# Kernel optimization log

Measured on AMD Instinct MI355X. Metric: run time of the kernel, lower is better.

## Reference

```python
import jax, jax.numpy as jnp
import numpy as np

T = 4      # num_step (also LSTM num_layers)
R = 64     # num_relation (= LSTM hidden size)
E = 1024   # num_entity
B = 128    # batch
IN = R + 2 * E  # LSTM input size


def _lstm_layer(x_seq, Wih, Whh, bih, bhh):
    # x_seq: [T, B, In]; torch gate order i, f, g, o
    Bsz = x_seq.shape[1]
    H = Whh.shape[1]
    pre = jnp.einsum('tbi,gi->tbg', x_seq, Wih) + bih + bhh  # [T,B,4H]

    def step(carry, z):
        h, c = carry
        z = z + h @ Whh.T
        i, f, g, o = jnp.split(z, 4, axis=-1)
        i, f, o = jax.nn.sigmoid(i), jax.nn.sigmoid(f), jax.nn.sigmoid(o)
        c = f * c + i * jnp.tanh(g)
        h = o * jnp.tanh(c)
        return (h, c), h

    init = (jnp.zeros((Bsz, H), x_seq.dtype), jnp.zeros((Bsz, H), x_seq.dtype))
    _, hs = jax.lax.scan(step, init, pre)
    return hs  # [T, B, H]


def setup_inputs() -> dict:
    key = jax.random.key(0)
    ks = jax.random.split(key, 12)
    s = 0.05
    inp = {
        'x': jax.random.uniform(ks[0], (B, IN), dtype=jnp.float32),
        'kb': jax.random.uniform(ks[1], (R, E, E), dtype=jnp.float32) * 0.01,
        # LSTM layer 0 (input dim IN)
        'Wih0': jax.random.normal(ks[2], (4 * R, IN), dtype=jnp.float32) * s,
        'Whh0': jax.random.normal(ks[3], (4 * R, R), dtype=jnp.float32) * s,
        'bih0': jnp.zeros((4 * R,), jnp.float32),
        'bhh0': jnp.zeros((4 * R,), jnp.float32),
        # LSTM layers 1..T-1 (input dim R)
        'Wih': jax.random.normal(ks[4], (T - 1, 4 * R, R), dtype=jnp.float32) * s,
        'Whh': jax.random.normal(ks[5], (T - 1, 4 * R, R), dtype=jnp.float32) * s,
        'bih': jnp.zeros((T - 1, 4 * R), jnp.float32),
        'bhh': jnp.zeros((T - 1, 4 * R), jnp.float32),
    }
    return inp


def reference(x, kb, Wih0, Whh0, bih0, bhh0, Wih, Whh, bih, bhh):
    # input to LSTM: x repeated T times -> [T, B, IN]
    seq = jnp.broadcast_to(x[None], (T,) + x.shape)
    hs = _lstm_layer(seq, Wih0, Whh0, bih0, bhh0)
    for l in range(T - 1):  # small fixed layer count
        hs = _lstm_layer(hs, Wih[l], Whh[l], bih[l], bhh[l])
    h = jax.nn.softmax(hs, axis=-1)  # [T, B, R] (first softmax)

    mem = [x[:, R:R + E]]  # memory[0] = head entity vector, [B, E]
    for i in range(T):
        h2 = jax.nn.softmax(h[i], axis=-1)  # double softmax, faithful to source
        # causal memory attention over steps k <= i
        att = jax.nn.softmax(jnp.einsum('kbr,br->bk', h[:i + 1], h[i]), axis=-1)  # [B, i+1]
        prev = jnp.einsum('bk,kbe->be', att, jnp.stack(mem))  # [B, E]
        # per-relation operator application: sum_r h2[b,r] * KB[r] @ prev[b]
        tmp = jnp.einsum('ref,bf->bre', kb, prev)  # [B, R, E]
        mem.append(jnp.einsum('br,bre->be', h2, tmp))

    tail = x[:, R + E:R + 2 * E]  # [B, E]
    score = jax.nn.sigmoid(-jnp.einsum('be,be->b', mem[-1], tail))[:, None]  # [B, 1]
    return score
```

## Files before the change

### kernel.cpp

```cpp
#include <hip/hip_runtime.h>
#include <cstdint>
#include <cstddef>

#define B_ 128
#define E_ 1024
#define R_ 64
#define T_ 4
#define IN_ 2112
#define G_ 256

typedef __attribute__((ext_vector_type(4))) float f32x4;
typedef __attribute__((ext_vector_type(8))) __bf16 bf16x8;

__device__ __forceinline__ unsigned short f2bf(float f) {
  unsigned int u = __float_as_uint(f);
  u += 0x7fffu + ((u >> 16) & 1u);
  return (unsigned short)(u >> 16);
}
__device__ __forceinline__ unsigned int pack2(float lo, float hi) {
  return (unsigned int)f2bf(lo) | ((unsigned int)f2bf(hi) << 16);
}
__device__ __forceinline__ float wred_sum(float v) {
#pragma unroll
  for (int m = 32; m > 0; m >>= 1) v += __shfl_xor(v, m, 64);
  return v;
}
__device__ __forceinline__ float wred_max(float v) {
#pragma unroll
  for (int m = 32; m > 0; m >>= 1) v = fmaxf(v, __shfl_xor(v, m, 64));
  return v;
}
__device__ __forceinline__ float fast_sig(float x) {
  return __builtin_amdgcn_rcpf(1.f + __expf(-x));
}
__device__ __forceinline__ float fast_tanh(float x) {
  return 1.f - 2.f * __builtin_amdgcn_rcpf(1.f + __expf(2.f * x));
}

__device__ __forceinline__ void gload_lds16(const void* g, void* l) {
  __builtin_amdgcn_global_load_lds(
      (const __attribute__((address_space(1))) unsigned int*)g,
      (__attribute__((address_space(3))) unsigned int*)l, 16, 0, 0);
}

__global__ __launch_bounds__(256) void fused0_kernel(
    const float* __restrict__ x, const float* __restrict__ kb,
    const float* __restrict__ Wih0, const float* __restrict__ Whh0,
    const float* __restrict__ bih0, const float* __restrict__ bhh0,
    const float* __restrict__ Wih, const float* __restrict__ Whh,
    const float* __restrict__ bih, const float* __restrict__ bhh,
    unsigned short* __restrict__ kb_bf,
    float* __restrict__ part,
    float* __restrict__ h2_out, float* __restrict__ att_out) {
  __shared__ __align__(16) unsigned char smem[20480];
  const int tid = threadIdx.x;
  const int bid = blockIdx.x;

  if (bid >= 128) {
    unsigned short* As = (unsigned short*)smem;
    unsigned short* Bs = As + 128 * 40;
    const int g = bid - 128;
    const int et = g & 7, r = g >> 3;
    const int row = tid >> 1;
    const int c0 = (tid & 1) * 16;
    const float* aptr = x + (size_t)row * IN_ + R_ + c0;
    const float* bptr = kb + (size_t)r * 1048576 + (size_t)(et * 128 + row) * 1024 + c0;
    unsigned short* kdst = kb_bf + (size_t)r * 1048576 + (size_t)(et * 128 + row) * 1024 + c0;
    unsigned short* adst = As + row * 40 + c0;
    unsigned short* bdst = Bs + row * 40 + c0;
    const int wv = tid >> 6, lane = tid & 63;
    const int wm = (wv & 1) * 64, wn = (wv >> 1) * 64;
    const int fr = lane & 15, koff = (lane >> 4) * 8;
    f32x4 acc[4][4];
#pragma unroll
    for (int mt = 0; mt < 4; mt++)
#pragma unroll
      for (int nt = 0; nt < 4; nt++)
#pragma unroll
        for (int q = 0; q < 4; q++) acc[mt][nt][q] = 0.f;

    for (int kk = 0; kk < 32; kk++) {
      const float4 a0 = *(const float4*)(aptr + kk * 32);
      const float4 a1 = *(const float4*)(aptr + kk * 32 + 4);
      const float4 a2 = *(const float4*)(aptr + kk * 32 + 8);
      const float4 a3 = *(const float4*)(aptr + kk * 32 + 12);
      const float4 b0 = *(const float4*)(bptr + kk * 32);
      const float4 b1 = *(const float4*)(bptr + kk * 32 + 4);
      const float4 b2 = *(const float4*)(bptr + kk * 32 + 8);
      const float4 b3 = *(const float4*)(bptr + kk * 32 + 12);
      __syncthreads();
      uint4 u;
      u.x = pack2(a0.x, a0.y); u.y = pack2(a0.z, a0.w);
      u.z = pack2(a1.x, a1.y); u.w = pack2(a1.z, a1.w);
      *(uint4*)adst = u;
      u.x = pack2(a2.x, a2.y); u.y = pack2(a2.z, a2.w);
      u.z = pack2(a3.x, a3.y); u.w = pack2(a3.z, a3.w);
      *(uint4*)(adst + 8) = u;
      uint4 ub;
      ub.x = pack2(b0.x, b0.y); ub.y = pack2(b0.z, b0.w);
      ub.z = pack2(b1.x, b1.y); ub.w = pack2(b1.z, b1.w);
      *(uint4*)bdst = ub;
      *(uint4*)(kdst + kk * 32) = ub;
      ub.x = pack2(b2.x, b2.y); ub.y = pack2(b2.z, b2.w);
      ub.z = pack2(b3.x, b3.y); ub.w = pack2(b3.z, b3.w);
      *(uint4*)(bdst + 8) = ub;
      *(uint4*)(kdst + kk * 32 + 8) = ub;
      __syncthreads();
      bf16x8 af[4], bfr[4];
#pragma unroll
      for (int mt = 0; mt < 4; mt++)
        af[mt] = *(const bf16x8*)(As + (wm + mt * 16 + fr) * 40 + koff);
#pragma unroll
      for (int nt = 0; nt < 4; nt++)
        bfr[nt] = *(const bf16x8*)(Bs + (wn + nt * 16 + fr) * 40 + koff);
#pragma unroll
      for (int mt = 0; mt < 4; mt++)
#pragma unroll
        for (int nt = 0; nt < 4; nt++)
          acc[mt][nt] = __builtin_amdgcn_mfma_f32_16x16x32_bf16(af[mt], bfr[nt], acc[mt][nt], 0, 0, 0);
    }
    const int crow = (lane >> 4) * 4;
    float* pout = part + (size_t)r * 131072;
#pragma unroll
    for (int mt = 0; mt < 4; mt++)
#pragma unroll
      for (int nt = 0; nt < 4; nt++)
#pragma unroll
        for (int q = 0; q < 4; q++)
          pout[(wm + mt * 16 + crow + q) * 1024 + et * 128 + wn + nt * 16 + fr] = acc[mt][nt][q];
    return;
  }

  float* xrow    = (float*)smem;
  float* pre_lds = xrow + IN_;
  float* hbuf    = pre_lds + G_;
  float* zbuf    = hbuf + R_;
  float* hs_out  = zbuf + 2 * G_;
  float* hmat    = hs_out + T_ * R_;

  const int b = bid;
  const int lane = tid & 63, wv = tid >> 6;
  const int s = tid & 63;

  for (int l = tid; l < IN_; l += 256) xrow[l] = x[b * IN_ + l];
  __syncthreads();

  {
    const int gbase = wv * 64;
#pragma unroll 2
    for (int gg = 0; gg < 64; gg++) {
      const float* wr = Wih0 + (size_t)(gbase + gg) * IN_;
      float4 s4 = {0.f, 0.f, 0.f, 0.f};
#pragma unroll
      for (int k = 0; k < 8; k++) {
        float4 w = *(const float4*)(wr + (lane + 64 * k) * 4);
        float4 xv = *(const float4*)(&xrow[(lane + 64 * k) * 4]);
        s4.x += w.x * xv.x; s4.y += w.y * xv.y;
        s4.z += w.z * xv.z; s4.w += w.w * xv.w;
      }
      float part_ = (s4.x + s4.y) + (s4.z + s4.w);
      part_ += wr[2048 + lane] * xrow[2048 + lane];
      float tot = wred_sum(part_);
      if (lane == 0) pre_lds[gbase + gg] = tot;
    }
  }
  float p0 = pre_lds[tid] + bih0[tid] + bhh0[tid];

  float4 w4[16];
  float pret[T_];

  auto scan = [&]() {
    __syncthreads();
    hbuf[s] = 0.f;
    float creg = 0.f;
#pragma unroll
    for (int t = 0; t < T_; t++) {
      float z0 = pret[t], z1 = 0.f, z2 = 0.f, z3 = 0.f;
#pragma unroll
      for (int q = 0; q < 16; q += 4) {
        float4 h0 = *(const float4*)(&hbuf[q * 4]);
        float4 h1 = *(const float4*)(&hbuf[q * 4 + 4]);
        float4 h2v = *(const float4*)(&hbuf[q * 4 + 8]);
        float4 h3 = *(const float4*)(&hbuf[q * 4 + 12]);
        z0 += h0.x * w4[q].x + h0.y * w4[q].y + h0.z * w4[q].z + h0.w * w4[q].w;
        z1 += h1.x * w4[q + 1].x + h1.y * w4[q + 1].y + h1.z * w4[q + 1].z + h1.w * w4[q + 1].w;
        z2 += h2v.x * w4[q + 2].x + h2v.y * w4[q + 2].y + h2v.z * w4[q + 2].z + h2v.w * w4[q + 2].w;
        z3 += h3.x * w4[q + 3].x + h3.y * w4[q + 3].y + h3.z * w4[q + 3].z + h3.w * w4[q + 3].w;
      }
      zbuf[(t & 1) * G_ + tid] = (z0 + z1) + (z2 + z3);
      __syncthreads();
      float iv = fast_sig(zbuf[(t & 1) * G_ + s]);
      float fv = fast_sig(zbuf[(t & 1) * G_ + R_ + s]);
      float gv = fast_tanh(zbuf[(t & 1) * G_ + 2 * R_ + s]);
      float ov = fast_sig(zbuf[(t & 1) * G_ + 3 * R_ + s]);
      creg = fv * creg + iv * gv;
      float h = ov * fast_tanh(creg);
      hbuf[s] = h;
      hs_out[t * R_ + s] = h;
    }
  };

#pragma unroll
  for (int t = 0; t < T_; t++) pret[t] = p0;
#pragma unroll
  for (int q = 0; q < 16; q++)
    w4[q] = *(const float4*)(Whh0 + (size_t)tid * R_ + q * 4);
  scan();

  for (int l = 0; l < T_ - 1; l++) {
#pragma unroll
    for (int q = 0; q < 16; q++)
      w4[q] = *(const float4*)(Wih + ((size_t)l * G_ + tid) * R_ + q * 4);
    const float bsum = bih[l * G_ + tid] + bhh[l * G_ + tid];
#pragma unroll
    for (int t = 0; t < T_; t++) {
      float p = bsum;
#pragma unroll
      for (int q = 0; q < 16; q++) {
        float4 hv = *(const float4*)(&hs_out[t * R_ + q * 4]);
        p += hv.x * w4[q].x + hv.y * w4[q].y + hv.z * w4[q].z + hv.w * w4[q].w;
      }
      pret[t] = p;
    }
#pragma unroll
    for (int q = 0; q < 16; q++)
      w4[q] = *(const float4*)(Whh + ((size_t)l * G_ + tid) * R_ + q * 4);
    scan();
  }

  {
    float v = hs_out[wv * R_ + lane];
    float mx = wred_max(v);
    float ev = expf(v - mx);
    float sm = wred_sum(ev);
    float hval = ev / sm;
    hmat[wv * R_ + lane] = hval;
    float mx2 = wred_max(hval);
    float e2 = expf(hval - mx2);
    float s2 = wred_sum(e2);
    h2_out[(wv * B_ + b) * R_ + lane] = e2 / s2;
    __syncthreads();
    float dots[T_];
    for (int k = 0; k <= wv; k++)
      dots[k] = wred_sum(hmat[k * R_ + lane] * hmat[wv * R_ + lane]);
    if (lane == 0) {
      float mx3 = dots[0];
      for (int k = 1; k <= wv; k++) mx3 = fmaxf(mx3, dots[k]);
      float ss = 0.f, es[T_];
      for (int k = 0; k <= wv; k++) { es[k] = expf(dots[k] - mx3); ss += es[k]; }
      for (int k = 0; k <= wv; k++) att_out[(wv * B_ + b) * 4 + k] = es[k] / ss;
    }
  }
}

__global__ __launch_bounds__(256) void gemm_bf_kernel(
    const unsigned short* __restrict__ Abf,
    const unsigned short* __restrict__ Kbf,
    float* __restrict__ part) {
  __shared__ unsigned short As[2][128 * 32];
  __shared__ unsigned short Bs[2][128 * 32];
  const int tid = threadIdx.x, wv = tid >> 6, lane = tid & 63;
  const int et = blockIdx.x, r = blockIdx.y;
  const int wm = (wv & 1) * 64, wn = (wv >> 1) * 64;
  const int fr = lane & 15, koff = (lane >> 4) * 8;

  const int srow = wv * 32 + (lane >> 2);
  const int scol = (lane & 3) * 8;
  const unsigned short* agp = Abf + (size_t)srow * 1024 + scol;
  const unsigned short* bgp = Kbf + (size_t)r * 1048576 + (size_t)(et * 128 + srow) * 1024 + scol;

  f32x4 acc[4][4];
#pragma unroll
  for (int mt = 0; mt < 4; mt++)
#pragma unroll
    for (int nt = 0; nt < 4; nt++)
#pragma unroll
      for (int q = 0; q < 4; q++) acc[mt][nt][q] = 0.f;

  auto stage = [&](int buf, int kk) {
    gload_lds16(agp + kk * 32,             As[buf] + wv * 1024);
    gload_lds16(agp + kk * 32 + 16 * 1024, As[buf] + wv * 1024 + 512);
    gload_lds16(bgp + kk * 32,             Bs[buf] + wv * 1024);
    gload_lds16(bgp + kk * 32 + 16 * 1024, Bs[buf] + wv * 1024 + 512);
  };

  stage(0, 0);
  __syncthreads();
  int cur = 0;
  for (int kk = 0; kk < 32; kk++) {
    if (kk < 31) stage(cur ^ 1, kk + 1);
    bf16x8 af[4], bfr[4];
#pragma unroll
    for (int mt = 0; mt < 4; mt++)
      af[mt] = *(const bf16x8*)(As[cur] + (wm + mt * 16 + fr) * 32 + koff);
#pragma unroll
    for (int nt = 0; nt < 4; nt++)
      bfr[nt] = *(const bf16x8*)(Bs[cur] + (wn + nt * 16 + fr) * 32 + koff);
#pragma unroll
    for (int mt = 0; mt < 4; mt++)
#pragma unroll
      for (int nt = 0; nt < 4; nt++)
        acc[mt][nt] = __builtin_amdgcn_mfma_f32_16x16x32_bf16(af[mt], bfr[nt], acc[mt][nt], 0, 0, 0);
    __syncthreads();
    cur ^= 1;
  }
  const int crow = (lane >> 4) * 4;
  float* pout = part + (size_t)r * 131072;
#pragma unroll
  for (int mt = 0; mt < 4; mt++)
#pragma unroll
    for (int nt = 0; nt < 4; nt++)
#pragma unroll
      for (int q = 0; q < 4; q++)
        pout[(wm + mt * 16 + crow + q) * 1024 + et * 128 + wn + nt * 16 + fr] = acc[mt][nt][q];
}

__global__ __launch_bounds__(256) void mid_kernel(
    const float* __restrict__ part, const float* __restrict__ h2,
    const float* __restrict__ att, const float* __restrict__ x,
    float* __restrict__ mem, unsigned short* __restrict__ prev_bf, int it) {
  const int idx = blockIdx.x * 256 + threadIdx.x;
  const int b = idx >> 10, e = idx & 1023;
  const float* h2row = h2 + (it * B_ + b) * R_;
  const float* pp = part + idx;
  float s = 0.f;
#pragma unroll 8
  for (int rr = 0; rr < 64; rr++) s += h2row[rr] * pp[(size_t)rr * 131072];
  mem[it * 131072 + idx] = s;
  if (it < 3) {
    const float* arow = att + ((it + 1) * B_ + b) * 4;
    float acc = arow[0] * x[b * IN_ + R_ + e];
    for (int k = 1; k <= it; k++) acc += arow[k] * mem[(k - 1) * 131072 + idx];
    acc += arow[it + 1] * s;
    prev_bf[idx] = f2bf(acc);
  }
}

__global__ __launch_bounds__(256) void prep_fp32_kernel(
    const float* __restrict__ x, const float* __restrict__ att,
    const float* __restrict__ mem, float* __restrict__ prev,
    float* __restrict__ newmem, int it) {
  const int idx = blockIdx.x * 256 + threadIdx.x;
  const int b = idx >> 10, e = idx & 1023;
  const float* arow = att + (it * B_ + b) * 4;
  float acc = arow[0] * x[b * IN_ + R_ + e];
  for (int k = 1; k <= it; k++)
    acc += arow[k] * mem[(k - 1) * (B_ * E_) + b * E_ + e];
  prev[idx] = acc;
  newmem[idx] = 0.f;
}

__global__ __launch_bounds__(256) void gemm_fp32_kernel(
    const float* __restrict__ prev, const float* __restrict__ h2,
    const float* __restrict__ kb, float* __restrict__ out) {
  __shared__ unsigned short As[128 * 40];
  __shared__ unsigned short Bs[128 * 40];
  __shared__ float h2s[128];
  const int tid = threadIdx.x;
  const int et = blockIdx.x;
  const int r = blockIdx.y;
  if (tid < 128) h2s[tid] = h2[tid * 64 + r];
  __syncthreads();
  const int row = tid >> 1;
  const int c0 = (tid & 1) * 16;
  const float hsc = h2s[row];
  const float* aptr = prev + row * 1024 + c0;
  const float* bptr = kb + (size_t)r * (1024u * 1024u) + (size_t)(et * 128 + row) * 1024 + c0;
  unsigned short* adst = As + row * 40 + c0;
  unsigned short* bdst = Bs + row * 40 + c0;
  const int wv = tid >> 6, lane = tid & 63;
  const int wm = (wv & 1) * 64, wn = (wv >> 1) * 64;
  const int fr = lane & 15, koff = (lane >> 4) * 8;
  f32x4 acc[4][4];
#pragma unroll
  for (int mt = 0; mt < 4; mt++)
#pragma unroll
    for (int nt = 0; nt < 4; nt++)
#pragma unroll
      for (int q = 0; q < 4; q++) acc[mt][nt][q] = 0.f;
  for (int kk = 0; kk < 32; kk++) {
    const float4 a0 = *(const float4*)(aptr + kk * 32);
    const float4 a1 = *(const float4*)(aptr + kk * 32 + 4);
    const float4 a2 = *(const float4*)(aptr + kk * 32 + 8);
    const float4 a3 = *(const float4*)(aptr + kk * 32 + 12);
    const float4 b0 = *(const float4*)(bptr + kk * 32);
    const float4 b1 = *(const float4*)(bptr + kk * 32 + 4);
    const float4 b2 = *(const float4*)(bptr + kk * 32 + 8);
    const float4 b3 = *(const float4*)(bptr + kk * 32 + 12);
    __syncthreads();
    uint4 u;
    u.x = pack2(a0.x * hsc, a0.y * hsc); u.y = pack2(a0.z * hsc, a0.w * hsc);
    u.z = pack2(a1.x * hsc, a1.y * hsc); u.w = pack2(a1.z * hsc, a1.w * hsc);
    *(uint4*)adst = u;
    u.x = pack2(a2.x * hsc, a2.y * hsc); u.y = pack2(a2.z * hsc, a2.w * hsc);
    u.z = pack2(a3.x * hsc, a3.y * hsc); u.w = pack2(a3.z * hsc, a3.w * hsc);
    *(uint4*)(adst + 8) = u;
    u.x = pack2(b0.x, b0.y); u.y = pack2(b0.z, b0.w);
    u.z = pack2(b1.x, b1.y); u.w = pack2(b1.z, b1.w);
    *(uint4*)bdst = u;
    u.x = pack2(b2.x, b2.y); u.y = pack2(b2.z, b2.w);
    u.z = pack2(b3.x, b3.y); u.w = pack2(b3.z, b3.w);
    *(uint4*)(bdst + 8) = u;
    __syncthreads();
    bf16x8 af[4], bfr[4];
#pragma unroll
    for (int mt = 0; mt < 4; mt++)
      af[mt] = *(const bf16x8*)(As + (wm + mt * 16 + fr) * 40 + koff);
#pragma unroll
    for (int nt = 0; nt < 4; nt++)
      bfr[nt] = *(const bf16x8*)(Bs + (wn + nt * 16 + fr) * 40 + koff);
#pragma unroll
    for (int mt = 0; mt < 4; mt++)
#pragma unroll
      for (int nt = 0; nt < 4; nt++)
        acc[mt][nt] = __builtin_amdgcn_mfma_f32_16x16x32_bf16(af[mt], bfr[nt], acc[mt][nt], 0, 0, 0);
  }
  const int crow = (lane >> 4) * 4;
  const int ccol = et * 128 + fr;
#pragma unroll
  for (int mt = 0; mt < 4; mt++)
#pragma unroll
    for (int nt = 0; nt < 4; nt++)
#pragma unroll
      for (int q = 0; q < 4; q++)
        atomicAdd(&out[(wm + mt * 16 + crow + q) * 1024 + ccol + wn + nt * 16], acc[mt][nt][q]);
}

__global__ __launch_bounds__(256) void score_kernel(
    const float* __restrict__ x, const float* __restrict__ mem4,
    float* __restrict__ out) {
  __shared__ float red[4];
  const int b = blockIdx.x, tid = threadIdx.x;
  float s = 0.f;
  for (int e = tid; e < E_; e += 256)
    s += mem4[b * E_ + e] * x[b * IN_ + R_ + E_ + e];
  s = wred_sum(s);
  if ((tid & 63) == 0) red[tid >> 6] = s;
  __syncthreads();
  if (tid == 0) {
    float t = red[0] + red[1] + red[2] + red[3];
    out[b] = 1.f / (1.f + expf(t));
  }
}

extern "C" void kernel_launch(void* const* d_in, const int* in_sizes, int n_in,
                              void* d_out, int out_size, void* d_ws, size_t ws_size,
                              hipStream_t stream) {
  const float* x    = (const float*)d_in[0];
  const float* kb   = (const float*)d_in[1];
  const float* Wih0 = (const float*)d_in[2];
  const float* Whh0 = (const float*)d_in[3];
  const float* bih0 = (const float*)d_in[4];
  const float* bhh0 = (const float*)d_in[5];
  const float* Wih  = (const float*)d_in[6];
  const float* Whh  = (const float*)d_in[7];
  const float* bih  = (const float*)d_in[8];
  const float* bhh  = (const float*)d_in[9];

  float* ws    = (float*)d_ws;
  float* h2    = ws;
  float* att   = ws + 32768;
  float* mem   = ws + 34816;
  float* prevb = ws + 559104;
  float* part  = ws + 690176;
  float* kbbf  = ws + 9078784;
  const size_t need_big = (size_t)(9078784 + 33554432) * sizeof(float);
  const bool big = ws_size >= need_big;

  if (big) {
    fused0_kernel<<<640, 256, 0, stream>>>(x, kb, Wih0, Whh0, bih0, bhh0,
                                           Wih, Whh, bih, bhh,
                                           (unsigned short*)kbbf, part, h2, att);
    mid_kernel<<<512, 256, 0, stream>>>(part, h2, att, x, mem,
                                        (unsigned short*)prevb, 0);
    for (int i = 1; i < 4; i++) {
      gemm_bf_kernel<<<dim3(8, 64), 256, 0, stream>>>(
          (const unsigned short*)prevb, (const unsigned short*)kbbf, part);
      mid_kernel<<<512, 256, 0, stream>>>(part, h2, att, x, mem,
                                          (unsigned short*)prevb, i);
    }
  } else {
    fused0_kernel<<<128, 256, 0, stream>>>(x, kb, Wih0, Whh0, bih0, bhh0,
                                           Wih, Whh, bih, bhh,
                                           (unsigned short*)prevb, mem, h2, att);
    for (int i = 0; i < 4; i++) {
      float* newmem = mem + i * (B_ * E_);
      prep_fp32_kernel<<<512, 256, 0, stream>>>(x, att, mem, prevb, newmem, i);
      gemm_fp32_kernel<<<dim3(8, 64), 256, 0, stream>>>(prevb, h2 + i * (B_ * R_), kb, newmem);
    }
  }
  score_kernel<<<128, 256, 0, stream>>>(x, mem + 3 * (B_ * E_), (float*)d_out);
}
```

Before: 609.4 us.

## Double-buffer fused kb conversion GEMM and halve gemm_bf N-tile for more blocks

The kb-conversion GEMM path in fused0_kernel now double-buffers its LDS tiles, prefetching the next global fp32 tile into registers while the MFMAs run and writing the converted bf16 tile afterwards, so one barrier per iteration replaces two. The gemm_bf_kernel N tile shrinks from 128 to 64 columns, doubling the grid to 1024 blocks for better CU occupancy. The cost is twice the LDS in fused0 and more re-reads of the A operand in the smaller-tile GEMM.

New measurement: 620.4 us. No clear change (+1.8%).

```diff
diff --git a/kernel.cpp b/kernel.cpp
--- a/kernel.cpp
+++ b/kernel.cpp
@@ -52,13 +52,13 @@
     unsigned short* __restrict__ kb_bf,
     float* __restrict__ part,
     float* __restrict__ h2_out, float* __restrict__ att_out) {
-  __shared__ __align__(16) unsigned char smem[20480];
+  __shared__ __align__(16) unsigned char smem[40960];
   const int tid = threadIdx.x;
   const int bid = blockIdx.x;
 
   if (bid >= 128) {
     unsigned short* As = (unsigned short*)smem;
-    unsigned short* Bs = As + 128 * 40;
+    unsigned short* Bs = As + 2 * 5120;
     const int g = bid - 128;
     const int et = g & 7, r = g >> 3;
     const int row = tid >> 1;
@@ -66,58 +66,71 @@
     const float* aptr = x + (size_t)row * IN_ + R_ + c0;
     const float* bptr = kb + (size_t)r * 1048576 + (size_t)(et * 128 + row) * 1024 + c0;
     unsigned short* kdst = kb_bf + (size_t)r * 1048576 + (size_t)(et * 128 + row) * 1024 + c0;
-    unsigned short* adst = As + row * 40 + c0;
-    unsigned short* bdst = Bs + row * 40 + c0;
     const int wv = tid >> 6, lane = tid & 63;
     const int wm = (wv & 1) * 64, wn = (wv >> 1) * 64;
     const int fr = lane & 15, koff = (lane >> 4) * 8;
-    f32x4 acc[4][4];
-#pragma unroll
-    for (int mt = 0; mt < 4; mt++)
-#pragma unroll
-      for (int nt = 0; nt < 4; nt++)
-#pragma unroll
-        for (int q = 0; q < 4; q++) acc[mt][nt][q] = 0.f;
-
-    for (int kk = 0; kk < 32; kk++) {
-      const float4 a0 = *(const float4*)(aptr + kk * 32);
-      const float4 a1 = *(const float4*)(aptr + kk * 32 + 4);
-      const float4 a2 = *(const float4*)(aptr + kk * 32 + 8);
-      const float4 a3 = *(const float4*)(aptr + kk * 32 + 12);
-      const float4 b0 = *(const float4*)(bptr + kk * 32);
-      const float4 b1 = *(const float4*)(bptr + kk * 32 + 4);
-      const float4 b2 = *(const float4*)(bptr + kk * 32 + 8);
-      const float4 b3 = *(const float4*)(bptr + kk * 32 + 12);
-      __syncthreads();
+
+    float4 ra0, ra1, ra2, ra3, rb0, rb1, rb2, rb3;
+    auto loadregs = [&](int kk) {
+      ra0 = *(const float4*)(aptr + kk * 32);
+      ra1 = *(const float4*)(aptr + kk * 32 + 4);
+      ra2 = *(const float4*)(aptr + kk * 32 + 8);
+      ra3 = *(const float4*)(aptr + kk * 32 + 12);
+      rb0 = *(const float4*)(bptr + kk * 32);
+      rb1 = *(const float4*)(bptr + kk * 32 + 4);
+      rb2 = *(const float4*)(bptr + kk * 32 + 8);
+      rb3 = *(const float4*)(bptr + kk * 32 + 12);
+    };
+    auto cvtwrite = [&](int buf, int kk) {
+      unsigned short* adst = As + buf * 5120 + row * 40 + c0;
+      unsigned short* bdst = Bs + buf * 5120 + row * 40 + c0;
       uint4 u;
-      u.x = pack2(a0.x, a0.y); u.y = pack2(a0.z, a0.w);
-      u.z = pack2(a1.x, a1.y); u.w = pack2(a1.z, a1.w);
+      u.x = pack2(ra0.x, ra0.y); u.y = pack2(ra0.z, ra0.w);
+      u.z = pack2(ra1.x, ra1.y); u.w = pack2(ra1.z, ra1.w);
       *(uint4*)adst = u;
-      u.x = pack2(a2.x, a2.y); u.y = pack2(a2.z, a2.w);
-      u.z = pack2(a3.x, a3.y); u.w = pack2(a3.z, a3.w);
+      u.x = pack2(ra2.x, ra2.y); u.y = pack2(ra2.z, ra2.w);
+      u.z = pack2(ra3.x, ra3.y); u.w = pack2(ra3.z, ra3.w);
       *(uint4*)(adst + 8) = u;
       uint4 ub;
-      ub.x = pack2(b0.x, b0.y); ub.y = pack2(b0.z, b0.w);
-      ub.z = pack2(b1.x, b1.y); ub.w = pack2(b1.z, b1.w);
+      ub.x = pack2(rb0.x, rb0.y); ub.y = pack2(rb0.z, rb0.w);
+      ub.z = pack2(rb1.x, rb1.y); ub.w = pack2(rb1.z, rb1.w);
       *(uint4*)bdst = ub;
       *(uint4*)(kdst + kk * 32) = ub;
-      ub.x = pack2(b2.x, b2.y); ub.y = pack2(b2.z, b2.w);
-      ub.z = pack2(b3.x, b3.y); ub.w = pack2(b3.z, b3.w);
+      ub.x = pack2(rb2.x, rb2.y); ub.y = pack2(rb2.z, rb2.w);
+      ub.z = pack2(rb3.x, rb3.y); ub.w = pack2(rb3.z, rb3.w);
       *(uint4*)(bdst + 8) = ub;
       *(uint4*)(kdst + kk * 32 + 8) = ub;
-      __syncthreads();
+    };
+
+    f32x4 acc[4][4];
+#pragma unroll
+    for (int mt = 0; mt < 4; mt++)
+#pragma unroll
+      for (int nt = 0; nt < 4; nt++)
+#pragma unroll
+        for (int q = 0; q < 4; q++) acc[mt][nt][q] = 0.f;
+
+    loadregs(0);
+    cvtwrite(0, 0);
+    __syncthreads();
+    int cur = 0;
+    for (int kk = 0; kk < 32; kk++) {
+      if (kk < 31) loadregs(kk + 1);
       bf16x8 af[4], bfr[4];
 #pragma unroll
       for (int mt = 0; mt < 4; mt++)
-        af[mt] = *(const bf16x8*)(As + (wm + mt * 16 + fr) * 40 + koff);
+        af[mt] = *(const bf16x8*)(As + cur * 5120 + (wm + mt * 16 + fr) * 40 + koff);
 #pragma unroll
       for (int nt = 0; nt < 4; nt++)
-        bfr[nt] = *(const bf16x8*)(Bs + (wn + nt * 16 + fr) * 40 + koff);
+        bfr[nt] = *(const bf16x8*)(Bs + cur * 5120 + (wn + nt * 16 + fr) * 40 + koff);
 #pragma unroll
       for (int mt = 0; mt < 4; mt++)
 #pragma unroll
         for (int nt = 0; nt < 4; nt++)
           acc[mt][nt] = __builtin_amdgcn_mfma_f32_16x16x32_bf16(af[mt], bfr[nt], acc[mt][nt], 0, 0, 0);
+      if (kk < 31) cvtwrite(cur ^ 1, kk + 1);
+      __syncthreads();
+      cur ^= 1;
     }
     const int crow = (lane >> 4) * 4;
     float* pout = part + (size_t)r * 131072;
@@ -258,30 +271,30 @@
     const unsigned short* __restrict__ Kbf,
     float* __restrict__ part) {
   __shared__ unsigned short As[2][128 * 32];
-  __shared__ unsigned short Bs[2][128 * 32];
+  __shared__ unsigned short Bs[2][64 * 32];
   const int tid = threadIdx.x, wv = tid >> 6, lane = tid & 63;
   const int et = blockIdx.x, r = blockIdx.y;
-  const int wm = (wv & 1) * 64, wn = (wv >> 1) * 64;
+  const int wm = (wv & 1) * 64, wn = (wv >> 1) * 32;
   const int fr = lane & 15, koff = (lane >> 4) * 8;
 
-  const int srow = wv * 32 + (lane >> 2);
+  const int srowA = wv * 32 + (lane >> 2);
+  const int srowB = wv * 16 + (lane >> 2);
   const int scol = (lane & 3) * 8;
-  const unsigned short* agp = Abf + (size_t)srow * 1024 + scol;
-  const unsigned short* bgp = Kbf + (size_t)r * 1048576 + (size_t)(et * 128 + srow) * 1024 + scol;
-
-  f32x4 acc[4][4];
+  const unsigned short* agp = Abf + (size_t)srowA * 1024 + scol;
+  const unsigned short* bgp = Kbf + (size_t)r * 1048576 + (size_t)(et * 64 + srowB) * 1024 + scol;
+
+  f32x4 acc[4][2];
 #pragma unroll
   for (int mt = 0; mt < 4; mt++)
 #pragma unroll
-    for (int nt = 0; nt < 4; nt++)
+    for (int nt = 0; nt < 2; nt++)
 #pragma unroll
       for (int q = 0; q < 4; q++) acc[mt][nt][q] = 0.f;
 
   auto stage = [&](int buf, int kk) {
     gload_lds16(agp + kk * 32,             As[buf] + wv * 1024);
     gload_lds16(agp + kk * 32 + 16 * 1024, As[buf] + wv * 1024 + 512);
-    gload_lds16(bgp + kk * 32,             Bs[buf] + wv * 1024);
-    gload_lds16(bgp + kk * 32 + 16 * 1024, Bs[buf] + wv * 1024 + 512);
+    gload_lds16(bgp + kk * 32,             Bs[buf] + wv * 512);
   };
 
   stage(0, 0);
@@ -289,17 +302,17 @@
   int cur = 0;
   for (int kk = 0; kk < 32; kk++) {
     if (kk < 31) stage(cur ^ 1, kk + 1);
-    bf16x8 af[4], bfr[4];
+    bf16x8 af[4], bfr[2];
 #pragma unroll
     for (int mt = 0; mt < 4; mt++)
       af[mt] = *(const bf16x8*)(As[cur] + (wm + mt * 16 + fr) * 32 + koff);
 #pragma unroll
-    for (int nt = 0; nt < 4; nt++)
+    for (int nt = 0; nt < 2; nt++)
       bfr[nt] = *(const bf16x8*)(Bs[cur] + (wn + nt * 16 + fr) * 32 + koff);
 #pragma unroll
     for (int mt = 0; mt < 4; mt++)
 #pragma unroll
-      for (int nt = 0; nt < 4; nt++)
+      for (int nt = 0; nt < 2; nt++)
         acc[mt][nt] = __builtin_amdgcn_mfma_f32_16x16x32_bf16(af[mt], bfr[nt], acc[mt][nt], 0, 0, 0);
     __syncthreads();
     cur ^= 1;
@@ -309,10 +322,10 @@
 #pragma unroll
   for (int mt = 0; mt < 4; mt++)
 #pragma unroll
-    for (int nt = 0; nt < 4; nt++)
+    for (int nt = 0; nt < 2; nt++)
 #pragma unroll
       for (int q = 0; q < 4; q++)
-        pout[(wm + mt * 16 + crow + q) * 1024 + et * 128 + wn + nt * 16 + fr] = acc[mt][nt][q];
+        pout[(wm + mt * 16 + crow + q) * 1024 + et * 64 + wn + nt * 16 + fr] = acc[mt][nt][q];
 }
 
 __global__ __launch_bounds__(256) void mid_kernel(
@@ -474,7 +487,7 @@
     mid_kernel<<<512, 256, 0, stream>>>(part, h2, att, x, mem,
                                         (unsigned short*)prevb, 0);
     for (int i = 1; i < 4; i++) {
-      gemm_bf_kernel<<<dim3(8, 64), 256, 0, stream>>>(
+      gemm_bf_kernel<<<dim3(16, 64), 256, 0, stream>>>(
           (const unsigned short*)prevb, (const unsigned short*)kbbf, part);
       mid_kernel<<<512, 256, 0, stream>>>(part, h2, att, x, mem,
                                           (unsigned short*)prevb, i);
```
